# Kernel optimization log

Hardware: AMD Instinct MI355X
Metric: run time of the kernel (lower is better)

The kernel has to match this reference:

```python
import jax, jax.numpy as jnp
import numpy as np

CHEB_K = 3  # diffusion_steps

def setup_inputs() -> dict:
    key = jax.random.key(0)
    k1, k2, k3 = jax.random.split(key, 3)
    N, D, B, C, O, K = 2048, 16, 64, 64, 64, CHEB_K
    node_embeddings = jax.random.normal(k1, (N, D), dtype=jnp.float32)
    feat = jax.random.normal(k2, (B, N, C), dtype=jnp.float32)
    # kaiming-uniform-like init for weights_pool, zeros bias (matches reset_parameters)
    fan_in = K * C  # fan_in of [D, K, C, O] per torch convention (dims after first)
    bound = 1.0 / np.sqrt(fan_in)
    weights_pool = jax.random.uniform(k3, (D, K, C, O), dtype=jnp.float32,
                                      minval=-bound, maxval=bound)
    bias_pool = jnp.zeros((D, O), dtype=jnp.float32)
    return {"node_embeddings": node_embeddings, "feat": feat,
            "weights_pool": weights_pool, "bias_pool": bias_pool}

def reference(node_embeddings, feat, weights_pool, bias_pool):
    N = node_embeddings.shape[0]
    K = weights_pool.shape[1]
    # adaptive adjacency: softmax(relu(E E^T)) row-wise
    sim = node_embeddings @ node_embeddings.T            # [N, N]
    supports = jax.nn.softmax(jax.nn.relu(sim), axis=1)  # [N, N]
    # Chebyshev polynomial recurrence: T0=I, T1=A, Tk = 2A Tk-1 - Tk-2
    support_set = [jnp.eye(N, dtype=supports.dtype), supports]
    for _ in range(2, K):
        support_set.append(2.0 * supports @ support_set[-1] - support_set[-2])
    supports_k = jnp.stack(support_set, axis=0)          # [K, N, N]
    # node-conditioned weights and bias
    weights = jnp.einsum('nd,dkio->nkio', node_embeddings, weights_pool)  # [N,K,C,O]
    bias = node_embeddings @ bias_pool                                    # [N, O]
    # graph diffusion of features
    x_g = jnp.einsum('knm,bmc->bknc', supports_k, feat)  # [B, K, N, C]
    x_g = jnp.transpose(x_g, (0, 2, 1, 3))               # [B, N, K, C]
    # per-node batched GEMM + bias
    x_gconv = jnp.einsum('bnki,nkio->bno', x_g, weights) + bias
    return x_gconv
```

## Files before the change

### kernel.cpp

```cpp
#include <hip/hip_runtime.h>
#include <stdint.h>

#define NN 2048
#define DE 16
#define BB 64
#define CC 64
#define OO 64
#define BC 4096
#define KR 192

using bf16x8 = __attribute__((ext_vector_type(8))) __bf16;
using f32x4  = __attribute__((ext_vector_type(4))) float;

__device__ __forceinline__ unsigned short f2bf(float f) {
  union { float f; unsigned int u; } v; v.f = f;
  unsigned int u = v.u;
  return (unsigned short)((u + 0x7FFFu + ((u >> 16) & 1u)) >> 16);
}
__device__ __forceinline__ float bf2f(unsigned short h) {
  union { unsigned int u; float f; } v; v.u = ((unsigned int)h) << 16;
  return v.f;
}
__device__ __forceinline__ void gll16(const void* g, void* l) {
  __builtin_amdgcn_global_load_lds(
      (const __attribute__((address_space(1))) unsigned int*)g,
      (__attribute__((address_space(3))) unsigned int*)l, 16, 0, 0);
}

__global__ __launch_bounds__(256) void prep(const float* __restrict__ feat,
                                            const float* __restrict__ E,
                                            const float* __restrict__ wp,
                                            const float* __restrict__ bp,
                                            unsigned short* __restrict__ Fbf,
                                            unsigned short* __restrict__ FbfT,
                                            unsigned short* __restrict__ Abf,
                                            float* __restrict__ Bias,
                                            unsigned short* __restrict__ Wg) {
  __shared__ float smem[64 * 65];
  const int id = blockIdx.x;
  const int t  = threadIdx.x;

  if (id < 2048) {
    float (*tile)[65] = (float (*)[65])smem;
    const int b  = id >> 5;
    const int n0 = (id & 31) * 64;
    const int tr = t >> 4, tc4 = (t & 15) * 4;
#pragma unroll
    for (int i = 0; i < 4; ++i) {
      const int r = tr + i * 16;
      const float4 v = *(const float4*)(feat + (size_t)b * (NN * CC) + (size_t)(n0 + r) * CC + tc4);
      tile[r][tc4 + 0] = v.x; tile[r][tc4 + 1] = v.y;
      tile[r][tc4 + 2] = v.z; tile[r][tc4 + 3] = v.w;
    }
    __syncthreads();
#pragma unroll
    for (int i = 0; i < 4; ++i) {
      const int r = tr + i * 16;
      const unsigned int lo = f2bf(tile[r][tc4 + 0]) | ((unsigned int)f2bf(tile[r][tc4 + 1]) << 16);
      const unsigned int hi = f2bf(tile[r][tc4 + 2]) | ((unsigned int)f2bf(tile[r][tc4 + 3]) << 16);
      *(uint2*)(Fbf + (size_t)(n0 + r) * BC + b * CC + tc4) = make_uint2(lo, hi);
    }
    const int rr = t & 63;
    const int cb = t >> 6;
#pragma unroll
    for (int i = 0; i < 16; ++i) {
      const int c = cb * 16 + i;
      FbfT[(size_t)(b * CC + c) * NN + n0 + rr] = f2bf(tile[rr][c]);
    }
  } else if (id < 4096) {
    const int n = id - 2048;
    float* en  = smem;
    float* red = smem + 16;
    if (t < 16) en[t] = E[n * 16 + t];
    __syncthreads();
    float er[16];
#pragma unroll
    for (int d = 0; d < 16; ++d) er[d] = en[d];

    float v[8];
    float mx = 0.0f;
#pragma unroll
    for (int i = 0; i < 8; ++i) {
      const int m = t + i * 256;
      const float4* Em = (const float4*)(E + m * 16);
      const float4 a = Em[0], b = Em[1], c = Em[2], d = Em[3];
      float dot = er[0] * a.x + er[1] * a.y + er[2] * a.z + er[3] * a.w
                + er[4] * b.x + er[5] * b.y + er[6] * b.z + er[7] * b.w
                + er[8] * c.x + er[9] * c.y + er[10] * c.z + er[11] * c.w
                + er[12] * d.x + er[13] * d.y + er[14] * d.z + er[15] * d.w;
      v[i] = fmaxf(dot, 0.0f);
      mx = fmaxf(mx, v[i]);
    }
#pragma unroll
    for (int off = 32; off > 0; off >>= 1) mx = fmaxf(mx, __shfl_xor(mx, off, 64));
    const int wave = t >> 6, lane = t & 63;
    if (lane == 0) red[wave] = mx;
    __syncthreads();
    mx = fmaxf(fmaxf(red[0], red[1]), fmaxf(red[2], red[3]));
    float s = 0.0f;
#pragma unroll
    for (int i = 0; i < 8; ++i) { v[i] = __expf(v[i] - mx); s += v[i]; }
#pragma unroll
    for (int off = 32; off > 0; off >>= 1) s += __shfl_xor(s, off, 64);
    if (lane == 0) red[4 + wave] = s;
    __syncthreads();
    s = red[4] + red[5] + red[6] + red[7];
    const float inv = 1.0f / s;
#pragma unroll
    for (int i = 0; i < 8; ++i)
      Abf[(size_t)n * NN + t + i * 256] = f2bf(v[i] * inv);
    if (t < 64) {
      float bs = 0.0f;
#pragma unroll
      for (int d = 0; d < 16; ++d) bs += er[d] * bp[d * 64 + t];
      Bias[n * 64 + t] = bs;
    }
  } else {
    const int wid = id - 4096;
    const int rq = wid % 24;
    const int nc = wid / 24;
    const int o  = t & 63;
    const int rh = (t >> 6) & 1;
    const int g  = t >> 7;
    float w[16][4];
#pragma unroll
    for (int d = 0; d < 16; ++d)
#pragma unroll
      for (int j = 0; j < 4; ++j)
        w[d][j] = wp[(size_t)d * (KR * OO) + (size_t)(rq * 8 + rh * 4 + j) * 64 + o];
    const int nbase = nc * 128 + g * 64;
    for (int i = 0; i < 64; ++i) {
      const int ns = __builtin_amdgcn_readfirstlane(nbase + i);
      const float* ep = E + ns * 16;
      float a0 = 0.f, a1 = 0.f, a2 = 0.f, a3 = 0.f;
#pragma unroll
      for (int d = 0; d < 16; ++d) {
        const float e = ep[d];
        a0 = fmaf(e, w[d][0], a0);
        a1 = fmaf(e, w[d][1], a1);
        a2 = fmaf(e, w[d][2], a2);
        a3 = fmaf(e, w[d][3], a3);
      }
      const unsigned int lo = f2bf(a0) | ((unsigned int)f2bf(a1) << 16);
      const unsigned int hi = f2bf(a2) | ((unsigned int)f2bf(a3) << 16);
      *(uint2*)(Wg + (size_t)ns * (KR * OO) + rq * 512 + o * 8 + rh * 4) = make_uint2(lo, hi);
    }
  }
}

template <int EPI>
__global__ __launch_bounds__(256, 2) void gemm128(const unsigned short* __restrict__ A,
                                                  const unsigned short* __restrict__ Bt,
                                                  unsigned short* __restrict__ Cnm,
                                                  unsigned short* __restrict__ Ct,
                                                  const unsigned short* __restrict__ F) {
  __shared__ alignas(16) unsigned short As[128 * 32];
  __shared__ alignas(16) unsigned short Bs[128 * 32];
  const int t = threadIdx.x;
  const int bm = blockIdx.y * 128, bn = blockIdx.x * 128;
  const int wave = t >> 6, lane = t & 63;
  const int wm = (wave >> 1) * 64, wn = (wave & 1) * 64;

  f32x4 acc[4][4];
#pragma unroll
  for (int r = 0; r < 4; ++r)
#pragma unroll
    for (int c = 0; c < 4; ++c) acc[r][c] = (f32x4){0.f, 0.f, 0.f, 0.f};

  const int r0 = t >> 2;
  const int csw = (((t & 3) ^ ((r0 >> 1) & 3)) * 8);
  const unsigned short* A0 = A + (size_t)(bm + r0) * NN + csw;
  const unsigned short* A1 = A + (size_t)(bm + r0 + 64) * NN + csw;
  const unsigned short* B0 = Bt + (size_t)(bn + r0) * NN + csw;
  const unsigned short* B1 = Bt + (size_t)(bn + r0 + 64) * NN + csw;
  const int e0 = t * 8, e1 = (t + 256) * 8;

  const int li = lane & 15, q = lane >> 4, sw = (li >> 1) & 3;
  const int aoff = (wm + li) * 32 + ((q ^ sw) * 8);
  const int boff = (wn + li) * 32 + ((q ^ sw) * 8);

  for (int k0 = 0; k0 < NN; k0 += 32) {
    __syncthreads();
    gll16(A0 + k0, &As[e0]);
    gll16(A1 + k0, &As[e1]);
    gll16(B0 + k0, &Bs[e0]);
    gll16(B1 + k0, &Bs[e1]);
    __syncthreads();
    bf16x8 af[4], bfr[4];
#pragma unroll
    for (int r = 0; r < 4; ++r) af[r] = *(const bf16x8*)&As[aoff + r * 512];
#pragma unroll
    for (int c = 0; c < 4; ++c) bfr[c] = *(const bf16x8*)&Bs[boff + c * 512];
#pragma unroll
    for (int r = 0; r < 4; ++r)
#pragma unroll
      for (int c = 0; c < 4; ++c)
        acc[r][c] = __builtin_amdgcn_mfma_f32_16x16x32_bf16(af[r], bfr[c], acc[r][c], 0, 0, 0);
  }

  const int colL = lane & 15, rowL = (lane >> 4) * 4;
#pragma unroll
  for (int r = 0; r < 4; ++r) {
#pragma unroll
    for (int c = 0; c < 4; ++c) {
      const int gm = bm + wm + r * 16 + rowL;
      const int gn = bn + wn + c * 16 + colL;
      const f32x4 a = acc[r][c];
      if (EPI == 1) {
#pragma unroll
        for (int i = 0; i < 4; ++i)
          Cnm[(size_t)(gm + i) * BC + gn] = f2bf(a[i]);
        const unsigned int lo = f2bf(a[0]) | ((unsigned int)f2bf(a[1]) << 16);
        const unsigned int hi = f2bf(a[2]) | ((unsigned int)f2bf(a[3]) << 16);
        *(uint2*)(Ct + (size_t)gn * NN + gm) = make_uint2(lo, hi);
      } else {
#pragma unroll
        for (int i = 0; i < 4; ++i) {
          const float g = 2.0f * a[i] - bf2f(F[(size_t)(gm + i) * BC + gn]);
          Cnm[(size_t)(gm + i) * BC + gn] = f2bf(g);
        }
      }
    }
  }
}

__global__ __launch_bounds__(256) void final_gemm(const unsigned short* __restrict__ Fbf,
                                                  const unsigned short* __restrict__ G1,
                                                  const unsigned short* __restrict__ G2,
                                                  const unsigned short* __restrict__ Wg,
                                                  const float* __restrict__ Bias,
                                                  float* __restrict__ out) {
  __shared__ alignas(16) unsigned short Xl[64 * 200];
  __shared__ alignas(16) unsigned short Wl[KR * OO];
  const int n = blockIdx.x, t = threadIdx.x;
  const unsigned short* srcs[3] = {Fbf + (size_t)n * BC, G1 + (size_t)n * BC, G2 + (size_t)n * BC};
#pragma unroll
  for (int kk = 0; kk < 3; ++kk) {
    const uint4* s = (const uint4*)srcs[kk];
    for (int p = t; p < 512; p += 256) {
      const uint4 v = s[p];
      const int j = p * 8, b = j >> 6, i = j & 63;
      *(uint4*)&Xl[b * 200 + kk * 64 + i] = v;
    }
  }
  {
    const uint4* s = (const uint4*)(Wg + (size_t)n * (KR * OO));
    uint4* d = (uint4*)Wl;
    for (int p = t; p < 1536; p += 256) d[p] = s[p];
  }
  __syncthreads();

  const int wave = t >> 6, lane = t & 63;
  const int q = lane >> 4;
  const int brow = wave * 16 + (lane & 15);
  f32x4 acc[4];
#pragma unroll
  for (int c = 0; c < 4; ++c) acc[c] = (f32x4){0.f, 0.f, 0.f, 0.f};
#pragma unroll
  for (int kq = 0; kq < 6; ++kq) {
    const bf16x8 a = *(const bf16x8*)&Xl[brow * 200 + kq * 32 + q * 8];
#pragma unroll
    for (int c = 0; c < 4; ++c) {
      const bf16x8 b = *(const bf16x8*)&Wl[(kq * 4 + q) * 512 + (c * 16 + (lane & 15)) * 8];
      acc[c] = __builtin_amdgcn_mfma_f32_16x16x32_bf16(a, b, acc[c], 0, 0, 0);
    }
  }
  const int col = lane & 15, rbase = wave * 16 + q * 4;
#pragma unroll
  for (int c = 0; c < 4; ++c) {
    const int o = c * 16 + col;
    const float bs = Bias[n * 64 + o];
#pragma unroll
    for (int i = 0; i < 4; ++i)
      out[(size_t)(rbase + i) * (NN * OO) + (size_t)n * OO + o] = acc[c][i] + bs;
  }
}

extern "C" void kernel_launch(void* const* d_in, const int* in_sizes, int n_in,
                              void* d_out, int out_size, void* d_ws, size_t ws_size,
                              hipStream_t stream) {
  const float* E    = (const float*)d_in[0];
  const float* feat = (const float*)d_in[1];
  const float* wp   = (const float*)d_in[2];
  const float* bp   = (const float*)d_in[3];
  float* out = (float*)d_out;

  char* ws = (char*)d_ws;
  size_t off = 0;
  auto alloc = [&](size_t bytes) -> void* {
    void* p = ws + off;
    off += (bytes + 255) & ~(size_t)255;
    return p;
  };
  unsigned short* Abf  = (unsigned short*)alloc((size_t)NN * NN * 2);
  unsigned short* FbfT = (unsigned short*)alloc((size_t)BC * NN * 2);
  unsigned short* Fbf  = (unsigned short*)alloc((size_t)NN * BC * 2);
  unsigned short* G1   = (unsigned short*)alloc((size_t)NN * BC * 2);
  unsigned short* G1T  = (unsigned short*)alloc((size_t)BC * NN * 2);
  unsigned short* Wg   = (unsigned short*)alloc((size_t)NN * KR * OO * 2);
  float* Bias          = (float*)alloc((size_t)NN * OO * 4);
  unsigned short* G2   = FbfT;

  prep<<<dim3(4480), 256, 0, stream>>>(feat, E, wp, bp, Fbf, FbfT, Abf, Bias, Wg);
  gemm128<1><<<dim3(32, 16), 256, 0, stream>>>(Abf, FbfT, G1, G1T, nullptr);
  gemm128<2><<<dim3(32, 16), 256, 0, stream>>>(Abf, G1T, G2, nullptr, Fbf);
  final_gemm<<<dim3(2048), 256, 0, stream>>>(Fbf, G1, G2, Wg, Bias, out);
}
```

Baseline: 239.7 us.

## Compute node weights with MFMA GEMM and deepen main GEMM K-tile to 64

The per-node weight generation (E @ weights_pool), previously done with scalar FMAs inside the prep kernel, now runs as a separate MFMA GEMM kernel. The prep kernel instead writes bf16 copies of E and a transposed bf16 weights_pool, and the MFMA pads K from 16 to 32 with zeros. Separately, the diffusion GEMM loads 64-wide K slices per stage with an 8-way swizzle, halving the number of barrier pairs per tile. This costs an extra kernel launch, bf16 rounding of E and wp before the product, and twice the LDS per block.

```diff
diff --git a/kernel.cpp b/kernel.cpp
--- a/kernel.cpp
+++ b/kernel.cpp
@@ -8,6 +8,7 @@
 #define OO 64
 #define BC 4096
 #define KR 192
+#define JJ 12288
 
 using bf16x8 = __attribute__((ext_vector_type(8))) __bf16;
 using f32x4  = __attribute__((ext_vector_type(4))) float;
@@ -35,7 +36,8 @@
                                             unsigned short* __restrict__ FbfT,
                                             unsigned short* __restrict__ Abf,
                                             float* __restrict__ Bias,
-                                            unsigned short* __restrict__ Wg) {
+                                            unsigned short* __restrict__ Ebf,
+                                            unsigned short* __restrict__ wpT2) {
   __shared__ float smem[64 * 65];
   const int id = blockIdx.x;
   const int t  = threadIdx.x;
@@ -73,6 +75,7 @@
     float* red = smem + 16;
     if (t < 16) en[t] = E[n * 16 + t];
     __syncthreads();
+    if (t < 16) Ebf[n * 16 + t] = f2bf(en[t]);
     float er[16];
 #pragma unroll
     for (int d = 0; d < 16; ++d) er[d] = en[d];
@@ -116,34 +119,68 @@
       Bias[n * 64 + t] = bs;
     }
   } else {
-    const int wid = id - 4096;
-    const int rq = wid % 24;
-    const int nc = wid / 24;
-    const int o  = t & 63;
-    const int rh = (t >> 6) & 1;
-    const int g  = t >> 7;
-    float w[16][4];
-#pragma unroll
-    for (int d = 0; d < 16; ++d)
-#pragma unroll
-      for (int j = 0; j < 4; ++j)
-        w[d][j] = wp[(size_t)d * (KR * OO) + (size_t)(rq * 8 + rh * 4 + j) * 64 + o];
-    const int nbase = nc * 128 + g * 64;
-    for (int i = 0; i < 64; ++i) {
-      const int ns = __builtin_amdgcn_readfirstlane(nbase + i);
-      const float* ep = E + ns * 16;
-      float a0 = 0.f, a1 = 0.f, a2 = 0.f, a3 = 0.f;
-#pragma unroll
-      for (int d = 0; d < 16; ++d) {
-        const float e = ep[d];
-        a0 = fmaf(e, w[d][0], a0);
-        a1 = fmaf(e, w[d][1], a1);
-        a2 = fmaf(e, w[d][2], a2);
-        a3 = fmaf(e, w[d][3], a3);
+    const int rq = id - 4096;
+    for (int p = t; p < 1024; p += 256) {
+      const int e0 = p * 8;
+      const int d0 = e0 & 15;
+      const int rem = e0 >> 4;
+      const int rl = rem & 7, o = rem >> 3;
+      const int r = rq * 8 + rl;
+      unsigned int w[4];
+#pragma unroll
+      for (int u = 0; u < 4; ++u) {
+        const float f0 = wp[(size_t)(d0 + 2 * u) * JJ + r * 64 + o];
+        const float f1 = wp[(size_t)(d0 + 2 * u + 1) * JJ + r * 64 + o];
+        w[u] = f2bf(f0) | ((unsigned int)f2bf(f1) << 16);
       }
-      const unsigned int lo = f2bf(a0) | ((unsigned int)f2bf(a1) << 16);
-      const unsigned int hi = f2bf(a2) | ((unsigned int)f2bf(a3) << 16);
-      *(uint2*)(Wg + (size_t)ns * (KR * OO) + rq * 512 + o * 8 + rh * 4) = make_uint2(lo, hi);
+      *(uint4*)(wpT2 + (size_t)rq * 8192 + e0) = make_uint4(w[0], w[1], w[2], w[3]);
+    }
+  }
+}
+
+__global__ __launch_bounds__(256) void make_w_mfma(const unsigned short* __restrict__ Ebf,
+                                                   const unsigned short* __restrict__ wpT2,
+                                                   unsigned short* __restrict__ Wg) {
+  __shared__ alignas(16) unsigned short As[128 * 16];
+  __shared__ alignas(16) unsigned short Bs[128 * 16];
+  const int t = threadIdx.x;
+  const int bm = blockIdx.y * 128;
+  const int bj = blockIdx.x * 128;
+  gll16(Ebf  + (size_t)(bm + (t >> 1)) * 16 + (t & 1) * 8, &As[t * 8]);
+  gll16(wpT2 + (size_t)(bj + (t >> 1)) * 16 + (t & 1) * 8, &Bs[t * 8]);
+  __syncthreads();
+  const int wave = t >> 6, lane = t & 63;
+  const int wm = (wave >> 1) * 64, wj = (wave & 1) * 64;
+  const int li = lane & 15, q = lane >> 4;
+  const bool hiK = (q >= 2);
+  const int qq = q & 1;
+  bf16x8 vz;
+#pragma unroll
+  for (int i = 0; i < 8; ++i) vz[i] = (__bf16)0.0f;
+
+  bf16x8 af[4], bfr[4];
+#pragma unroll
+  for (int r = 0; r < 4; ++r) {
+    af[r] = *(const bf16x8*)&As[(wm + r * 16 + li) * 16 + qq * 8];
+    if (hiK) af[r] = vz;
+  }
+#pragma unroll
+  for (int c = 0; c < 4; ++c) {
+    bfr[c] = *(const bf16x8*)&Bs[(wj + c * 16 + li) * 16 + qq * 8];
+    if (hiK) bfr[c] = vz;
+  }
+  const int rowL = q * 4;
+#pragma unroll
+  for (int r = 0; r < 4; ++r) {
+#pragma unroll
+    for (int c = 0; c < 4; ++c) {
+      f32x4 acc = (f32x4){0.f, 0.f, 0.f, 0.f};
+      acc = __builtin_amdgcn_mfma_f32_16x16x32_bf16(af[r], bfr[c], acc, 0, 0, 0);
+      const int gm = bm + wm + r * 16 + rowL;
+      const int gj = bj + wj + c * 16 + li;
+#pragma unroll
+      for (int i = 0; i < 4; ++i)
+        Wg[(size_t)(gm + i) * JJ + gj] = f2bf(acc[i]);
     }
   }
 }
@@ -154,8 +191,8 @@
                                                   unsigned short* __restrict__ Cnm,
                                                   unsigned short* __restrict__ Ct,
                                                   const unsigned short* __restrict__ F) {
-  __shared__ alignas(16) unsigned short As[128 * 32];
-  __shared__ alignas(16) unsigned short Bs[128 * 32];
+  __shared__ alignas(16) unsigned short As[128 * 64];
+  __shared__ alignas(16) unsigned short Bs[128 * 64];
   const int t = threadIdx.x;
   const int bm = blockIdx.y * 128, bn = blockIdx.x * 128;
   const int wave = t >> 6, lane = t & 63;
@@ -167,35 +204,40 @@
 #pragma unroll
     for (int c = 0; c < 4; ++c) acc[r][c] = (f32x4){0.f, 0.f, 0.f, 0.f};
 
-  const int r0 = t >> 2;
-  const int csw = (((t & 3) ^ ((r0 >> 1) & 3)) * 8);
-  const unsigned short* A0 = A + (size_t)(bm + r0) * NN + csw;
-  const unsigned short* A1 = A + (size_t)(bm + r0 + 64) * NN + csw;
-  const unsigned short* B0 = Bt + (size_t)(bn + r0) * NN + csw;
-  const unsigned short* B1 = Bt + (size_t)(bn + r0 + 64) * NN + csw;
-  const int e0 = t * 8, e1 = (t + 256) * 8;
-
-  const int li = lane & 15, q = lane >> 4, sw = (li >> 1) & 3;
-  const int aoff = (wm + li) * 32 + ((q ^ sw) * 8);
-  const int boff = (wn + li) * 32 + ((q ^ sw) * 8);
-
-  for (int k0 = 0; k0 < NN; k0 += 32) {
-    __syncthreads();
-    gll16(A0 + k0, &As[e0]);
-    gll16(A1 + k0, &As[e1]);
-    gll16(B0 + k0, &Bs[e0]);
-    gll16(B1 + k0, &Bs[e1]);
-    __syncthreads();
-    bf16x8 af[4], bfr[4];
-#pragma unroll
-    for (int r = 0; r < 4; ++r) af[r] = *(const bf16x8*)&As[aoff + r * 512];
-#pragma unroll
-    for (int c = 0; c < 4; ++c) bfr[c] = *(const bf16x8*)&Bs[boff + c * 512];
-#pragma unroll
-    for (int r = 0; r < 4; ++r)
+  const int srow = t >> 3;
+  const int csw = (((t & 7) ^ ((t >> 4) & 7)) * 8);
+  const unsigned short* Ap[4];
+  const unsigned short* Bp[4];
+#pragma unroll
+  for (int i = 0; i < 4; ++i) {
+    Ap[i] = A  + (size_t)(bm + srow + i * 32) * NN + csw;
+    Bp[i] = Bt + (size_t)(bn + srow + i * 32) * NN + csw;
+  }
+  const int li = lane & 15, q = lane >> 4, sw = (li >> 1) & 7;
+  const int arow = (wm + li) * 64, brow = (wn + li) * 64;
+
+  for (int k0 = 0; k0 < NN; k0 += 64) {
+    __syncthreads();
+#pragma unroll
+    for (int i = 0; i < 4; ++i) gll16(Ap[i] + k0, &As[(t + i * 256) * 8]);
+#pragma unroll
+    for (int i = 0; i < 4; ++i) gll16(Bp[i] + k0, &Bs[(t + i * 256) * 8]);
+    __syncthreads();
+#pragma unroll
+    for (int kk = 0; kk < 2; ++kk) {
+      bf16x8 af[4], bfr[4];
+#pragma unroll
+      for (int r = 0; r < 4; ++r)
+        af[r] = *(const bf16x8*)&As[arow + r * 16 * 64 + (((kk * 4 + q) ^ sw) * 8)];
 #pragma unroll
       for (int c = 0; c < 4; ++c)
-        acc[r][c] = __builtin_amdgcn_mfma_f32_16x16x32_bf16(af[r], bfr[c], acc[r][c], 0, 0, 0);
+        bfr[c] = *(const bf16x8*)&Bs[brow + c * 16 * 64 + (((kk * 4 + q) ^ sw) * 8)];
+#pragma unroll
+      for (int r = 0; r < 4; ++r)
+#pragma unroll
+        for (int c = 0; c < 4; ++c)
+          acc[r][c] = __builtin_amdgcn_mfma_f32_16x16x32_bf16(af[r], bfr[c], acc[r][c], 0, 0, 0);
+    }
   }
 
   const int colL = lane & 15, rowL = (lane >> 4) * 4;
@@ -244,7 +286,7 @@
     }
   }
   {
-    const uint4* s = (const uint4*)(Wg + (size_t)n * (KR * OO));
+    const uint4* s = (const uint4*)(Wg + (size_t)n * JJ);
     uint4* d = (uint4*)Wl;
     for (int p = t; p < 1536; p += 256) d[p] = s[p];
   }
@@ -297,11 +339,14 @@
   unsigned short* Fbf  = (unsigned short*)alloc((size_t)NN * BC * 2);
   unsigned short* G1   = (unsigned short*)alloc((size_t)NN * BC * 2);
   unsigned short* G1T  = (unsigned short*)alloc((size_t)BC * NN * 2);
-  unsigned short* Wg   = (unsigned short*)alloc((size_t)NN * KR * OO * 2);
+  unsigned short* Wg   = (unsigned short*)alloc((size_t)NN * JJ * 2);
   float* Bias          = (float*)alloc((size_t)NN * OO * 4);
+  unsigned short* Ebf  = (unsigned short*)alloc((size_t)NN * DE * 2);
+  unsigned short* wpT2 = (unsigned short*)alloc((size_t)JJ * DE * 2);
   unsigned short* G2   = FbfT;
 
-  prep<<<dim3(4480), 256, 0, stream>>>(feat, E, wp, bp, Fbf, FbfT, Abf, Bias, Wg);
+  prep<<<dim3(4120), 256, 0, stream>>>(feat, E, wp, bp, Fbf, FbfT, Abf, Bias, Ebf, wpT2);
+  make_w_mfma<<<dim3(96, 16), 256, 0, stream>>>(Ebf, wpT2, Wg);
   gemm128<1><<<dim3(32, 16), 256, 0, stream>>>(Abf, FbfT, G1, G1T, nullptr);
   gemm128<2><<<dim3(32, 16), 256, 0, stream>>>(Abf, G1T, G2, nullptr, Fbf);
   final_gemm<<<dim3(2048), 256, 0, stream>>>(Fbf, G1, G2, Wg, Bias, out);
```

Result: faster. 219.5 us (-8.4%).
